# Kernel tuning notes

Hardware: AMD Instinct MI355X
Metric: run time of the kernel (lower is better)

The kernel has to match this reference:

```python
import jax, jax.numpy as jnp
import numpy as np

DIM = 1024
NUM_HEADS = 16
HEAD_DIM = DIM // NUM_HEADS
INNER_ITR = 4
INNER_LR = 1.0
SCALE_QKV = 1.0


def setup_inputs() -> dict:
    key = jax.random.key(0)
    k1, k2, k3 = jax.random.split(key, 3)
    B, N, C = 8, 1024, DIM
    x = jax.random.normal(k1, (B, N, C), dtype=jnp.float32)
    # Xavier-uniform-ish scaled dense kernels
    w_qkv = jax.random.normal(k2, (C, 3 * C), dtype=jnp.float32) * (1.0 / np.sqrt(C))
    w_proj = jax.random.normal(k3, (C, C), dtype=jnp.float32) * (1.0 / np.sqrt(C))
    b_proj = jnp.zeros((C,), dtype=jnp.float32)
    return {"x": x, "w_qkv": w_qkv, "w_proj": w_proj, "b_proj": b_proj, "training": 0}


def _mttt_base(q, k, v):
    """MTTT 'base' inner loop: per (B,H) linear model W,b trained by
    INNER_ITR full-batch GD steps on MSE reconstruction of v from k,
    then applied to q. Shapes: q,k,v are (B, H, N, d)."""
    B, H, N, d = q.shape
    W = jnp.zeros((B, H, d, d), dtype=q.dtype)
    b = jnp.zeros((B, H, 1, d), dtype=q.dtype)
    invN = 1.0 / N
    for _ in range(INNER_ITR):  # small fixed iteration count
        pred = jnp.einsum('bhnd,bhde->bhne', k, W) + b   # (B,H,N,d)
        err = pred - v
        gW = jnp.einsum('bhnd,bhne->bhde', k, err) * invN
        gb = jnp.mean(err, axis=2, keepdims=True)
        W = W - INNER_LR * gW
        b = b - INNER_LR * gb
    return jnp.einsum('bhnd,bhde->bhne', q, W) + b       # (B,H,N,d)


def reference(x, w_qkv, w_proj, b_proj, training):
    B, N, C = x.shape
    H, d = NUM_HEADS, HEAD_DIM
    qkv = jnp.einsum('bnc,ce->bne', x, w_qkv)            # (B,N,3C), qkv_bias=False
    qkv = qkv.reshape(B, N, 3, H, d).transpose(2, 0, 3, 1, 4)  # (3,B,H,N,d)
    qkv = qkv * SCALE_QKV
    q, k, v = qkv[0], qkv[1], qkv[2]
    # qk_norm=False -> identity; scale_q=False -> no q scaling
    out = _mttt_base(q, k, v)                            # (B,H,N,d)
    out = out.transpose(0, 2, 1, 3).reshape(B, N, C)
    out = jnp.einsum('bnc,cd->bnd', out, w_proj) + b_proj
    # proj dropout deterministic (training=False)
    return out
```

## Files before the change

kernel.cpp:

```cpp
#include <hip/hip_runtime.h>


#define SEQ    1024
#define NBATCH 8
#define DIMC   1024
#define NHEAD  16
#define HDIM   64
#define MROWS  8192
#define NQKV   3072

typedef __attribute__((ext_vector_type(8))) __bf16 bf16x8;
typedef __attribute__((ext_vector_type(4))) float  f32x4;

__device__ __forceinline__ unsigned short f2b(float f) {
  union { float f; unsigned int u; } v; v.f = f;
  unsigned int r = (v.u + 0x7FFFu + ((v.u >> 16) & 1u)) >> 16;
  return (unsigned short)r;
}

__device__ __forceinline__ void load_lds16(const void* g, void* l) {
  __builtin_amdgcn_global_load_lds(
      (__attribute__((address_space(1))) void*)(void*)(g),
      (__attribute__((address_space(3))) void*)(l), 16, 0, 0);
}

#define FENCE asm volatile("" ::: "memory")
#define BAR   __builtin_amdgcn_s_barrier()

__global__ __launch_bounds__(256) void prep(const float* __restrict__ x,
                                            const float* __restrict__ wq,
                                            const float* __restrict__ wp,
                                            unsigned short* __restrict__ xb,
                                            unsigned short* __restrict__ wqT,
                                            unsigned short* __restrict__ wpT) {
  __shared__ unsigned short tile[32][33];
  const int bid = blockIdx.x, tid = threadIdx.x;
  if (bid < 8192) {
    int i = bid * 256 + tid;
    float4 v = ((const float4*)x)[i];
    ushort4 o;
    o.x = f2b(v.x); o.y = f2b(v.y); o.z = f2b(v.z); o.w = f2b(v.w);
    ((ushort4*)xb)[i] = o;
    return;
  }
  const float* in; unsigned short* out; int R, Cc, tix;
  if (bid < 8192 + 3072) { tix = bid - 8192; in = wq; out = wqT; R = 1024; Cc = 3072; }
  else                   { tix = bid - 8192 - 3072; in = wp; out = wpT; R = 1024; Cc = 1024; }
  const int nbx = Cc / 32;
  const int c0 = (tix % nbx) * 32, r0 = (tix / nbx) * 32;
  const int tx = tid & 31, ty = tid >> 5;
  for (int i = ty; i < 32; i += 8)
    tile[i][tx] = f2b(in[(size_t)(r0 + i) * Cc + c0 + tx]);
  __syncthreads();
  for (int i = ty; i < 32; i += 8)
    out[(size_t)(c0 + i) * R + r0 + tx] = tile[tx][i];
}

template <int BM, int BN, int WM, int WN, int ASTRIDE, int BMODE, int PERB>
__device__ __forceinline__
void gemm_r3(const unsigned short* __restrict__ A,
             const unsigned short* __restrict__ BT,
             void* __restrict__ Cout,
             const float* __restrict__ bias,
             int N, int NBN) {
  constexpr int THREADS = WM * WN * 64;
  constexpr int MF      = BM / (WM * 16);
  constexpr int NF      = BN / (WN * 16);
  constexpr int TR      = THREADS / 4;
  constexpr int ABYTES  = BM * 64;
  constexpr int TBYTES  = (BM + BN) * 64;
  constexpr int CALLS   = TBYTES / (THREADS * 16);
  constexpr int NT      = 32;

  extern __shared__ __align__(16) char ldsb[];

  const int tid  = threadIdx.x;
  const int lane = tid & 63, wave = tid >> 6;
  const int wr = wave / WN, wc = wave % WN;
  const int frow = lane & 15, g4 = lane >> 4;
  const int cz = (g4 ^ ((frow >> 1) & 3)) * 16;

  const int cpx = gridDim.x >> 3;
  const int wg  = (blockIdx.x & 7) * cpx + (blockIdx.x >> 3);
  const int bm = wg / NBN, bn = wg % NBN;
  const size_t m0 = (size_t)bm * BM, n0 = (size_t)bn * BN;

  const unsigned short* BTb = PERB ? (BT + (m0 >> 10) * (size_t)(1024 * 1024)) : BT;

  const int trow = tid >> 2;
  const int scol = ((tid & 3) ^ ((tid >> 3) & 3)) * 8;
  const unsigned short* psrc[CALLS];
#pragma unroll
  for (int c = 0; c < CALLS; ++c) {
    const int rr = c * TR + trow;
    psrc[c] = (rr < BM) ? (A + (m0 + rr) * (size_t)ASTRIDE + scol)
                        : (BTb + (size_t)(n0 + rr - BM) * 1024 + scol);
  }

  f32x4 acc[MF][NF];
  if (BMODE == 2) {
    const float* bp = bias + (m0 >> 10) * (size_t)N;
#pragma unroll
    for (int j = 0; j < NF; ++j) {
      float4 bv = *(const float4*)&bp[n0 + wc * (BN / WN) + j * 16 + g4 * 4];
      f32x4 t; t[0] = bv.x; t[1] = bv.y; t[2] = bv.z; t[3] = bv.w;
#pragma unroll
      for (int i = 0; i < MF; ++i) acc[i][j] = t;
    }
  } else {
#pragma unroll
    for (int i = 0; i < MF; ++i)
#pragma unroll
      for (int j = 0; j < NF; ++j) acc[i][j] = f32x4{0.f, 0.f, 0.f, 0.f};
  }

  auto stage = [&](int tk, int buf) {
    char* base = ldsb + buf * TBYTES + wave * 1024;
#pragma unroll
    for (int c = 0; c < CALLS; ++c)
      load_lds16(psrc[c] + tk * 32, base + c * (THREADS * 16));
  };

  const int aoff = (wr * (BM / WM) + frow) * 64 + cz;
  const int boff = ABYTES + (wc * (BN / WN) + frow) * 64 + cz;

  stage(0, 0); stage(1, 1);
  asm volatile("s_waitcnt vmcnt(%0)" :: "i"(CALLS) : "memory");
  FENCE; BAR;

  int bcur = 0, bpre = 2;
#pragma unroll 1
  for (int t = 0; t < NT; ++t) {
    if (t + 2 < NT) stage(t + 2, bpre);
    const char* rb = ldsb + bcur * TBYTES;
    bf16x8 af[MF], bq[NF];
#pragma unroll
    for (int i = 0; i < MF; ++i) af[i] = *(const bf16x8*)(rb + aoff + i * 1024);
#pragma unroll
    for (int j = 0; j < NF; ++j) bq[j] = *(const bf16x8*)(rb + boff + j * 1024);
#pragma unroll
    for (int i = 0; i < MF; ++i)
#pragma unroll
      for (int j = 0; j < NF; ++j)
        acc[i][j] = __builtin_amdgcn_mfma_f32_16x16x32_bf16(bq[j], af[i],
                                                            acc[i][j], 0, 0, 0);
    if (t + 2 < NT) asm volatile("s_waitcnt vmcnt(%0)" :: "i"(CALLS) : "memory");
    else            asm volatile("s_waitcnt vmcnt(0)" ::: "memory");
    FENCE; BAR;
    bcur = (bcur == 2) ? 0 : bcur + 1;
    bpre = (bpre == 2) ? 0 : bpre + 1;
  }

  const size_t mbase = m0 + wr * (BM / WM) + frow;
  const size_t nbase = n0 + wc * (BN / WN) + g4 * 4;
  if (BMODE == 2) {
    float* C = (float*)Cout;
#pragma unroll
    for (int i = 0; i < MF; ++i)
#pragma unroll
      for (int j = 0; j < NF; ++j) {
        float4 o; o.x = acc[i][j][0]; o.y = acc[i][j][1];
        o.z = acc[i][j][2]; o.w = acc[i][j][3];
        *(float4*)&C[(mbase + i * 16) * N + nbase + j * 16] = o;
      }
  } else {
    unsigned short* C = (unsigned short*)Cout;
#pragma unroll
    for (int i = 0; i < MF; ++i)
#pragma unroll
      for (int j = 0; j < NF; ++j) {
        ushort4 o; o.x = f2b(acc[i][j][0]); o.y = f2b(acc[i][j][1]);
        o.z = f2b(acc[i][j][2]); o.w = f2b(acc[i][j][3]);
        *(ushort4*)&C[(mbase + i * 16) * N + nbase + j * 16] = o;
      }
  }
}

__global__ __launch_bounds__(512, 4) void g_qkv(const unsigned short* __restrict__ A,
                                                const unsigned short* __restrict__ BT,
                                                void* __restrict__ C,
                                                const float* __restrict__ bias, int N, int NBN) {
  gemm_r3<128, 256, 2, 4, 1024, 0, 0>(A, BT, C, bias, N, NBN);
}
__global__ __launch_bounds__(256, 3) void g_out(const unsigned short* __restrict__ A,
                                                const unsigned short* __restrict__ BT,
                                                void* __restrict__ C,
                                                const float* __restrict__ bias, int N, int NBN) {
  gemm_r3<128, 128, 2, 2, NQKV, 2, 1>(A, BT, C, bias, N, NBN);
}

__global__ __launch_bounds__(256) void stats_part(const unsigned short* __restrict__ qkvb,
                                                  float* __restrict__ spart) {
  __shared__ __align__(16) char smem[51200];
  unsigned short (*kd)[72] = (unsigned short(*)[72])(smem);
  unsigned short (*vd)[72] = (unsigned short(*)[72])(smem + 9216);
  char* knb = smem + 18432;
  char* vnb = smem + 34816;

  const int bh2 = blockIdx.x;
  const int bh = bh2 >> 1, half = bh2 & 1;
  const int b = bh >> 4, h = bh & 15;
  const int tid = threadIdx.x;
  const int lane = tid & 63, wave = tid >> 6;
  const int frow = lane & 15;
  const int fk = (lane >> 4) * 8;

  const unsigned short* kg = qkvb + (size_t)b * 1024 * 3072 + 1024 + h * 64;
  const unsigned short* vg = qkvb + (size_t)b * 1024 * 3072 + 2048 + h * 64;

  typedef __attribute__((ext_vector_type(8))) unsigned short u16x8;
  u16x8 onesu = {0x3F80, 0x3F80, 0x3F80, 0x3F80, 0x3F80, 0x3F80, 0x3F80, 0x3F80};
  const bf16x8 ones = __builtin_bit_cast(bf16x8, onesu);

  f32x4 accG[4], accP[4], accK1, accV1;
#pragma unroll
  for (int j = 0; j < 4; ++j) {
    accG[j] = f32x4{0.f, 0.f, 0.f, 0.f};
    accP[j] = f32x4{0.f, 0.f, 0.f, 0.f};
  }
  accK1 = f32x4{0.f, 0.f, 0.f, 0.f};
  accV1 = f32x4{0.f, 0.f, 0.f, 0.f};

  const size_t srcn = (size_t)(tid >> 3) * 3072 + (tid & 7) * 8;
  const int td = tid & 63, tng = tid >> 6;

  auto issue = [&](int ch, int buf) {
    const size_t nb0 = (size_t)half * 512 + (size_t)ch * 64;
#pragma unroll
    for (int c = 0; c < 2; ++c) {
      load_lds16(kg + (nb0 + 32 * c) * 3072 + srcn, knb + buf * 8192 + c * 4096 + wave * 1024);
      load_lds16(vg + (nb0 + 32 * c) * 3072 + srcn, vnb + buf * 8192 + c * 4096 + wave * 1024);
    }
  };

  issue(0, 0);
#pragma unroll 1
  for (int ch = 0; ch < 8; ++ch) {
    if (ch + 1 < 8) {
      issue(ch + 1, (ch + 1) & 1);
      asm volatile("s_waitcnt vmcnt(4)" ::: "memory");
    } else {
      asm volatile("s_waitcnt vmcnt(0)" ::: "memory");
    }
    FENCE; BAR;
    {
      const unsigned short (*kn)[64] = (const unsigned short(*)[64])(knb + (ch & 1) * 8192);
      const unsigned short (*vn)[64] = (const unsigned short(*)[64])(vnb + (ch & 1) * 8192);
      alignas(16) unsigned short pk[16], pv[16];
#pragma unroll
      for (int j = 0; j < 16; ++j) {
        pk[j] = kn[tng * 16 + j][td];
        pv[j] = vn[tng * 16 + j][td];
      }
      *(uint4*)&kd[td][tng * 16]     = *(const uint4*)pk;
      *(uint4*)&kd[td][tng * 16 + 8] = *(const uint4*)(pk + 8);
      *(uint4*)&vd[td][tng * 16]     = *(const uint4*)pv;
      *(uint4*)&vd[td][tng * 16 + 8] = *(const uint4*)(pv + 8);
    }
    FENCE; BAR;
#pragma unroll
    for (int ks = 0; ks < 2; ++ks) {
      const int nb = ks * 32 + fk;
      bf16x8 afk = *(const bf16x8*)&kd[wave * 16 + frow][nb];
      bf16x8 afv = *(const bf16x8*)&vd[wave * 16 + frow][nb];
      bf16x8 kf[4], vf[4];
#pragma unroll
      for (int j = 0; j < 4; ++j) {
        kf[j] = *(const bf16x8*)&kd[j * 16 + frow][nb];
        vf[j] = *(const bf16x8*)&vd[j * 16 + frow][nb];
      }
#pragma unroll
      for (int j = 0; j < 4; ++j) {
        accG[j] = __builtin_amdgcn_mfma_f32_16x16x32_bf16(afk, kf[j], accG[j], 0, 0, 0);
        accP[j] = __builtin_amdgcn_mfma_f32_16x16x32_bf16(afk, vf[j], accP[j], 0, 0, 0);
      }
      accK1 = __builtin_amdgcn_mfma_f32_16x16x32_bf16(afk, ones, accK1, 0, 0, 0);
      accV1 = __builtin_amdgcn_mfma_f32_16x16x32_bf16(afv, ones, accV1, 0, 0, 0);
    }
    FENCE; BAR;
  }

  float* dst = spart + (size_t)bh2 * 40 * 256;
#pragma unroll
  for (int j = 0; j < 4; ++j)
#pragma unroll
    for (int r = 0; r < 4; ++r) dst[(j * 4 + r) * 256 + tid] = accG[j][r];
#pragma unroll
  for (int j = 0; j < 4; ++j)
#pragma unroll
    for (int r = 0; r < 4; ++r) dst[(16 + j * 4 + r) * 256 + tid] = accP[j][r];
#pragma unroll
  for (int r = 0; r < 4; ++r) dst[(32 + r) * 256 + tid] = accK1[r];
#pragma unroll
  for (int r = 0; r < 4; ++r) dst[(36 + r) * 256 + tid] = accV1[r];
}

__global__ __launch_bounds__(256) void gd_wc(const float* __restrict__ spart,
                                             const unsigned short* __restrict__ wpT,
                                             unsigned short* __restrict__ WcT,
                                             float* __restrict__ bvec) {
  __shared__ __align__(16) char smem[52224];
  float (*Gs)[68] = (float(*)[68])(smem);
  float (*Ps)[68] = (float(*)[68])(smem + 17408);
  float (*Ws)[68] = (float(*)[68])(smem + 34816);
  unsigned short (*wb16)[72] = (unsigned short(*)[72])(smem);
  __shared__ float mks[64], mvs[64], bs[64];

  const int bh = blockIdx.x, b = bh >> 4, h = bh & 15;
  const int tid = threadIdx.x;
  const int lane = tid & 63, wave = tid >> 6;
  const int frow = lane & 15, g4 = lane >> 4, fk = g4 * 8;

  const float* s0 = spart + (size_t)(bh * 2) * 40 * 256;
  const float* s1 = spart + (size_t)(bh * 2 + 1) * 40 * 256;
  float fsum[40];
#pragma unroll
  for (int w = 0; w < 40; ++w) fsum[w] = s0[w * 256 + tid] + s1[w * 256 + tid];

  const float invN = 1.0f / (float)SEQ;
  const int orow = wave * 16 + (lane >> 4) * 4;
#pragma unroll
  for (int j = 0; j < 4; ++j)
#pragma unroll
    for (int r = 0; r < 4; ++r) {
      Gs[orow + r][j * 16 + frow] = fsum[j * 4 + r] * invN;
      Ps[orow + r][j * 16 + frow] = fsum[16 + j * 4 + r] * invN;
    }
  if (frow == 0) {
#pragma unroll
    for (int r = 0; r < 4; ++r) {
      mks[orow + r] = fsum[32 + r] * invN;
      mvs[orow + r] = fsum[36 + r] * invN;
    }
  }
  const int r = tid >> 2;
  const int c0 = (tid & 3) * 16;
  if (tid < 64) bs[tid] = 0.f;
#pragma unroll
  for (int c = 0; c < 16; ++c) Ws[r][c0 + c] = 0.f;
  __syncthreads();

  for (int it = 0; it < 4; ++it) {
    float wn[16];
#pragma unroll
    for (int c = 0; c < 16; ++c)
      wn[c] = Ws[r][c0 + c] + Ps[r][c0 + c] - mks[r] * bs[c0 + c];
    for (int j = 0; j < 64; ++j) {
      float g = Gs[r][j];
#pragma unroll
      for (int c = 0; c < 16; ++c) wn[c] -= g * Ws[j][c0 + c];
    }
    float bn = 0.f;
    if (tid < 64) {
      bn = mvs[tid];
      for (int j = 0; j < 64; ++j) bn -= mks[j] * Ws[j][tid];
    }
    __syncthreads();
#pragma unroll
    for (int c = 0; c < 16; ++c) Ws[r][c0 + c] = wn[c];
    if (tid < 64) bs[tid] = bn;
    __syncthreads();
  }

  if (tid < 64) bvec[(size_t)bh * HDIM + tid] = bs[tid];

#pragma unroll
  for (int c = 0; c < 16; ++c)
    wb16[r][c0 + c] = f2b(Ws[r][c0 + c]);
  __syncthreads();

  unsigned short* dstb = WcT + (size_t)b * 1024 * 1024;
#pragma unroll 1
  for (int pblk = 0; pblk < 4; ++pblk) {
    const int p0 = pblk * 256 + wave * 64;
    f32x4 acc[4][4];
#pragma unroll
    for (int i = 0; i < 4; ++i)
#pragma unroll
      for (int j = 0; j < 4; ++j) acc[i][j] = f32x4{0.f, 0.f, 0.f, 0.f};
#pragma unroll
    for (int kk = 0; kk < 2; ++kk) {
      bf16x8 af[4], bq[4];
#pragma unroll
      for (int i = 0; i < 4; ++i)
        af[i] = *(const bf16x8*)&wpT[(size_t)(p0 + i * 16 + frow) * 1024 + h * 64 + kk * 32 + fk];
#pragma unroll
      for (int j = 0; j < 4; ++j)
        bq[j] = *(const bf16x8*)&wb16[j * 16 + frow][kk * 32 + fk];
#pragma unroll
      for (int i = 0; i < 4; ++i)
#pragma unroll
        for (int j = 0; j < 4; ++j)
          acc[i][j] = __builtin_amdgcn_mfma_f32_16x16x32_bf16(bq[j], af[i], acc[i][j], 0, 0, 0);
    }
#pragma unroll
    for (int i = 0; i < 4; ++i)
#pragma unroll
      for (int j = 0; j < 4; ++j) {
        ushort4 o; o.x = f2b(acc[i][j][0]); o.y = f2b(acc[i][j][1]);
        o.z = f2b(acc[i][j][2]); o.w = f2b(acc[i][j][3]);
        *(ushort4*)&dstb[(size_t)(p0 + i * 16 + frow) * 1024 + h * 64 + j * 16 + g4 * 4] = o;
      }
  }
}

__global__ __launch_bounds__(256) void bc_part(const float* __restrict__ wp,
                                               const float* __restrict__ bvec,
                                               float* __restrict__ part) {
  const int p  = blockIdx.x * 256 + threadIdx.x;
  const int cc = blockIdx.y;
  float s[8];
#pragma unroll
  for (int b = 0; b < 8; ++b) s[b] = 0.f;
  const int c0 = cc * 64;
  for (int c = c0; c < c0 + 64; ++c) {
    float w = wp[(size_t)c * 1024 + p];
#pragma unroll
    for (int b = 0; b < 8; ++b) s[b] += bvec[b * 1024 + c] * w;
  }
  float* dst = part + (size_t)cc * 8192;
#pragma unroll
  for (int b = 0; b < 8; ++b) dst[b * 1024 + p] = s[b];
}

__global__ __launch_bounds__(256) void bc_reduce(const float* __restrict__ part,
                                                 const float* __restrict__ b_proj,
                                                 float* __restrict__ bc) {
  const int idx = blockIdx.x * 256 + threadIdx.x;
  const int p = idx & 1023;
  float s = b_proj[p];
#pragma unroll
  for (int cc = 0; cc < 16; ++cc) s += part[(size_t)cc * 8192 + idx];
  bc[idx] = s;
}

extern "C" void kernel_launch(void* const* d_in, const int* in_sizes, int n_in,
                              void* d_out, int out_size, void* d_ws, size_t ws_size,
                              hipStream_t stream) {
  const float* x      = (const float*)d_in[0];
  const float* w_qkv  = (const float*)d_in[1];
  const float* w_proj = (const float*)d_in[2];
  const float* b_proj = (const float*)d_in[3];

  char* ws = (char*)d_ws;
  unsigned short* xb    = (unsigned short*)(ws + 0);
  float*          spart = (float*)(ws + 0);
  unsigned short* wqT   = (unsigned short*)(ws + 16777216);
  unsigned short* wpT   = (unsigned short*)(ws + 23068672);
  unsigned short* qkvb  = (unsigned short*)(ws + 25165824);
  unsigned short* WcT   = (unsigned short*)(ws + 109051904);
  float*          bvec  = (float*)(ws + 126877696);
  float*          bc    = (float*)(ws + 126910464);
  float*          bpart = (float*)(ws + 126943232);
  if (ws_size < (size_t)127467520) return;

  hipFuncSetAttribute((const void*)g_qkv, hipFuncAttributeMaxDynamicSharedMemorySize, 73728);
  hipFuncSetAttribute((const void*)g_out, hipFuncAttributeMaxDynamicSharedMemorySize, 49152);

  prep<<<dim3(8192 + 3072 + 1024), 256, 0, stream>>>(x, w_qkv, w_proj, xb, wqT, wpT);
  g_qkv<<<dim3(768), dim3(512), 73728, stream>>>(xb, wqT, qkvb, nullptr, NQKV, 12);
  stats_part<<<256, 256, 0, stream>>>(qkvb, spart);
  gd_wc<<<128, 256, 0, stream>>>(spart, wpT, WcT, bvec);
  bc_part<<<dim3(4, 16), 256, 0, stream>>>(w_proj, bvec, bpart);
  bc_reduce<<<32, 256, 0, stream>>>(bpart, b_proj, bc);
  g_out<<<dim3(512), dim3(256), 49152, stream>>>(qkvb, WcT, d_out, bc, DIMC, 8);
}
```

Baseline: 166.0 us.

## Fuse bias partial reduction into output GEMM and simplify stats_part loads

Removes the bc_reduce kernel launch by having the output GEMM sum the 16 bias partials plus b_proj directly when it initializes its accumulators. Separately, stats_part drops its double-buffered async K/V prefetch for a single-buffer load-wait-compute loop, and the padded transposed tiles widen from 72 to 136 columns. The fusion saves a launch and a round trip through global memory, but each GEMM block now re-reads the partials redundantly. The stats_part change gives up load/compute overlap, and the wider kd/vd rows may not match the unseen compute code.

```diff
diff --git a/kernel.cpp b/kernel.cpp
--- a/kernel.cpp
+++ b/kernel.cpp
@@ -62,6 +62,7 @@
              const unsigned short* __restrict__ BT,
              void* __restrict__ Cout,
              const float* __restrict__ bias,
+             const float* __restrict__ part,
              int N, int NBN) {
   constexpr int THREADS = WM * WN * 64;
   constexpr int MF      = BM / (WM * 16);
@@ -98,11 +99,17 @@
   }
 
   f32x4 acc[MF][NF];
-  if (BMODE == 2) {
-    const float* bp = bias + (m0 >> 10) * (size_t)N;
+  if (BMODE == 3) {
+    const int bb = (int)(m0 >> 10);
 #pragma unroll
     for (int j = 0; j < NF; ++j) {
-      float4 bv = *(const float4*)&bp[n0 + wc * (BN / WN) + j * 16 + g4 * 4];
+      const int p0 = (int)n0 + wc * (BN / WN) + j * 16 + g4 * 4;
+      float4 bv = *(const float4*)&bias[p0];
+#pragma unroll
+      for (int cc = 0; cc < 16; ++cc) {
+        float4 pv = *(const float4*)&part[(size_t)cc * 8192 + bb * 1024 + p0];
+        bv.x += pv.x; bv.y += pv.y; bv.z += pv.z; bv.w += pv.w;
+      }
       f32x4 t; t[0] = bv.x; t[1] = bv.y; t[2] = bv.z; t[3] = bv.w;
 #pragma unroll
       for (int i = 0; i < MF; ++i) acc[i][j] = t;
@@ -153,7 +160,7 @@
 
   const size_t mbase = m0 + wr * (BM / WM) + frow;
   const size_t nbase = n0 + wc * (BN / WN) + g4 * 4;
-  if (BMODE == 2) {
+  if (BMODE == 3) {
     float* C = (float*)Cout;
 #pragma unroll
     for (int i = 0; i < MF; ++i)
@@ -179,23 +186,25 @@
 __global__ __launch_bounds__(512, 4) void g_qkv(const unsigned short* __restrict__ A,
                                                 const unsigned short* __restrict__ BT,
                                                 void* __restrict__ C,
-                                                const float* __restrict__ bias, int N, int NBN) {
-  gemm_r3<128, 256, 2, 4, 1024, 0, 0>(A, BT, C, bias, N, NBN);
+                                                int N, int NBN) {
+  gemm_r3<128, 256, 2, 4, 1024, 0, 0>(A, BT, C, nullptr, nullptr, N, NBN);
 }
 __global__ __launch_bounds__(256, 3) void g_out(const unsigned short* __restrict__ A,
                                                 const unsigned short* __restrict__ BT,
                                                 void* __restrict__ C,
-                                                const float* __restrict__ bias, int N, int NBN) {
-  gemm_r3<128, 128, 2, 2, NQKV, 2, 1>(A, BT, C, bias, N, NBN);
+                                                const float* __restrict__ b_proj,
+                                                const float* __restrict__ bpart,
+                                                int N, int NBN) {
+  gemm_r3<128, 128, 2, 2, NQKV, 3, 1>(A, BT, C, b_proj, bpart, N, NBN);
 }
 
 __global__ __launch_bounds__(256) void stats_part(const unsigned short* __restrict__ qkvb,
                                                   float* __restrict__ spart) {
   __shared__ __align__(16) char smem[51200];
-  unsigned short (*kd)[72] = (unsigned short(*)[72])(smem);
-  unsigned short (*vd)[72] = (unsigned short(*)[72])(smem + 9216);
-  char* knb = smem + 18432;
-  char* vnb = smem + 34816;
+  unsigned short (*kd)[136] = (unsigned short(*)[136])(smem);
+  unsigned short (*vd)[136] = (unsigned short(*)[136])(smem + 17408);
+  unsigned short (*kn)[64]  = (unsigned short(*)[64])(smem + 34816);
+  unsigned short (*vn)[64]  = (unsigned short(*)[64])(smem + 43008);
 
   const int bh2 = blockIdx.x;
   const int bh = bh2 >> 1, half = bh2 & 1;
@@ -224,28 +233,16 @@
   const size_t srcn = (size_t)(tid >> 3) * 3072 + (tid & 7) * 8;
   const int td = tid & 63, tng = tid >> 6;
 
-  auto issue = [&](int ch, int buf) {
+  for (int ch = 0; ch < 8; ++ch) {
     const size_t nb0 = (size_t)half * 512 + (size_t)ch * 64;
 #pragma unroll
     for (int c = 0; c < 2; ++c) {
-      load_lds16(kg + (nb0 + 32 * c) * 3072 + srcn, knb + buf * 8192 + c * 4096 + wave * 1024);
-      load_lds16(vg + (nb0 + 32 * c) * 3072 + srcn, vnb + buf * 8192 + c * 4096 + wave * 1024);
-    }
-  };
-
-  issue(0, 0);
-#pragma unroll 1
-  for (int ch = 0; ch < 8; ++ch) {
-    if (ch + 1 < 8) {
-      issue(ch + 1, (ch + 1) & 1);
-      asm volatile("s_waitcnt vmcnt(4)" ::: "memory");
-    } else {
-      asm volatile("s_waitcnt vmcnt(0)" ::: "memory");
-    }
+      load_lds16(kg + (nb0 + 32 * c) * 3072 + srcn, (char*)kn + c * 4096 + wave * 1024);
+      load_lds16(vg + (nb0 + 32 * c) * 3072 + srcn, (char*)vn + c * 4096 + wave * 1024);
+    }
+    asm volatile("s_waitcnt vmcnt(0)" ::: "memory");
     FENCE; BAR;
     {
-      const unsigned short (*kn)[64] = (const unsigned short(*)[64])(knb + (ch & 1) * 8192);
-      const unsigned short (*vn)[64] = (const unsigned short(*)[64])(vnb + (ch & 1) * 8192);
       alignas(16) unsigned short pk[16], pv[16];
 #pragma unroll
       for (int j = 0; j < 16; ++j) {
@@ -423,17 +420,6 @@
   for (int b = 0; b < 8; ++b) dst[b * 1024 + p] = s[b];
 }
 
-__global__ __launch_bounds__(256) void bc_reduce(const float* __restrict__ part,
-                                                 const float* __restrict__ b_proj,
-                                                 float* __restrict__ bc) {
-  const int idx = blockIdx.x * 256 + threadIdx.x;
-  const int p = idx & 1023;
-  float s = b_proj[p];
-#pragma unroll
-  for (int cc = 0; cc < 16; ++cc) s += part[(size_t)cc * 8192 + idx];
-  bc[idx] = s;
-}
-
 extern "C" void kernel_launch(void* const* d_in, const int* in_sizes, int n_in,
                               void* d_out, int out_size, void* d_ws, size_t ws_size,
                               hipStream_t stream) {
@@ -450,7 +436,6 @@
   unsigned short* qkvb  = (unsigned short*)(ws + 25165824);
   unsigned short* WcT   = (unsigned short*)(ws + 109051904);
   float*          bvec  = (float*)(ws + 126877696);
-  float*          bc    = (float*)(ws + 126910464);
   float*          bpart = (float*)(ws + 126943232);
   if (ws_size < (size_t)127467520) return;
 
@@ -458,10 +443,9 @@
   hipFuncSetAttribute((const void*)g_out, hipFuncAttributeMaxDynamicSharedMemorySize, 49152);
 
   prep<<<dim3(8192 + 3072 + 1024), 256, 0, stream>>>(x, w_qkv, w_proj, xb, wqT, wpT);
-  g_qkv<<<dim3(768), dim3(512), 73728, stream>>>(xb, wqT, qkvb, nullptr, NQKV, 12);
+  g_qkv<<<dim3(768), dim3(512), 73728, stream>>>(xb, wqT, qkvb, NQKV, 12);
   stats_part<<<256, 256, 0, stream>>>(qkvb, spart);
   gd_wc<<<128, 256, 0, stream>>>(spart, wpT, WcT, bvec);
   bc_part<<<dim3(4, 16), 256, 0, stream>>>(w_proj, bvec, bpart);
-  bc_reduce<<<32, 256, 0, stream>>>(bpart, b_proj, bc);
-  g_out<<<dim3(512), dim3(256), 49152, stream>>>(qkvb, WcT, d_out, bc, DIMC, 8);
-}
+  g_out<<<dim3(512), dim3(256), 49152, stream>>>(qkvb, WcT, d_out, b_proj, bpart, DIMC, 8);
+}
```

Result: slower. 169.8 us (+2.3%).
